# Performance work log

Measured on AMD Instinct MI355X. Metric: run time of the kernel, lower is better.

Reference implementation:

```python
import jax, jax.numpy as jnp
import numpy as np

INF = 1000000000.0
N_HEAD, QK, VD, NVAR = 4, 4, 4, 1


def _rope(xh, tf, thetas):
    # xh: [B, L, H, D], tf: [B, L], thetas: [D//2]
    freqs = tf[:, :, None] * thetas                     # [B, L, D//2]
    cos = jnp.cos(freqs)[:, :, None, :]                 # broadcast over heads
    sin = jnp.sin(freqs)[:, :, None, :]
    xr, xi = xh[..., 0::2], xh[..., 1::2]               # complex pairs
    out_r = xr * cos - xi * sin
    out_i = xr * sin + xi * cos
    return jnp.stack([out_r, out_i], axis=-1).reshape(xh.shape)


def setup_inputs() -> dict:
    key = jax.random.key(0)
    ks = jax.random.split(key, 11)
    bn, pn, pl = 32, 64, 128
    s = 0.1
    return {
        "x": jax.random.normal(ks[0], (bn, pn, pl), jnp.float32),
        "t": jax.random.uniform(ks[1], (bn, pn, pl), jnp.float32),
        "mask": jax.random.randint(ks[2], (bn, pn, pl), 0, 2, jnp.int32),
        "Wq": jax.random.normal(ks[3], (N_HEAD * QK, NVAR), jnp.float32) * s,
        "Wk": jax.random.normal(ks[4], (N_HEAD * QK, NVAR), jnp.float32) * s,
        "Wv": jax.random.normal(ks[5], (N_HEAD * VD, NVAR), jnp.float32) * s,
        "Wout": jax.random.normal(ks[6], (NVAR, N_HEAD * VD), jnp.float32) * s,
        "W1": jax.random.normal(ks[7], (4 * N_HEAD * VD, N_HEAD * VD), jnp.float32) * s,
        "b1": jnp.zeros((4 * N_HEAD * VD,), jnp.float32),
        "W2": jax.random.normal(ks[8], (N_HEAD * VD, 4 * N_HEAD * VD), jnp.float32) * s,
        "b2": jnp.zeros((N_HEAD * VD,), jnp.float32),
    }


def reference(x, t, mask, Wq, Wk, Wv, Wout, W1, b1, W2, b2):
    bn, pn, pl = x.shape
    B = bn * pn
    thetas = 1.0 / (1000.0 ** (jnp.arange(0, QK, 2, dtype=jnp.float32) / QK))
    x4 = x[..., None]                                       # [bn, pn, pl, 1]
    q = jnp.einsum('bpln,dn->bpld', x4, Wq).reshape(B, pl, N_HEAD, QK)
    k = jnp.einsum('bpln,dn->bpld', x4, Wk).reshape(B, pl, N_HEAD, QK)
    v = jnp.einsum('bpln,dn->bpld', x4, Wv).reshape(B, pl, N_HEAD, VD)
    tf = t.reshape(B, pl)
    q = _rope(q, tf, thetas)
    k = _rope(k, tf, thetas)
    q = q.transpose(0, 2, 1, 3)                             # [B, H, L, D]
    k = k.transpose(0, 2, 1, 3)
    v = v.transpose(0, 2, 1, 3)
    scale = QK ** 0.5
    attn = jnp.einsum('bhqd,bhkd->bhqk', q / scale, k)      # [B, H, L, L]
    m = mask.reshape(B, pl)
    mask_mat = (m[:, :, None] * m[:, None, :])[:, None, :, :]
    attn = jnp.where(mask_mat == 0, -INF, attn)
    attn = jax.nn.softmax(attn, axis=-1)
    o = jnp.einsum('bhqk,bhkd->bhqd', attn, v)
    o = o.transpose(0, 2, 1, 3).reshape(bn, pn, pl, N_HEAD * VD)
    ffn = jnp.maximum(o @ W1.T + b1, 0.0) @ W2.T + b2       # dropout off (eval)
    out_q = o + ffn
    return out_q @ Wout.T                                   # [bn, pn, pl, 1]
```

## Files before the change

kernel.cpp:

```cpp
#include <hip/hip_runtime.h>

constexpr int PL = 128;

typedef float f32x2 __attribute__((ext_vector_type(2)));

__device__ __forceinline__ float fast_exp2(float x) {
#if __has_builtin(__builtin_amdgcn_exp2f)
    return __builtin_amdgcn_exp2f(x);
#else
    return __expf(x * 0.69314718055994531f);
#endif
}
__device__ __forceinline__ f32x2 pk_fma(f32x2 a, f32x2 b, f32x2 c) {
    return __builtin_elementwise_fma(a, b, c);
}
__device__ __forceinline__ f32x2 sp(float v) { f32x2 r; r.x = v; r.y = v; return r; }

__global__ __launch_bounds__(256, 4) void fused_block_kernel(
    const float* __restrict__ x, const float* __restrict__ t, const int* __restrict__ mask,
    const float* __restrict__ Wq, const float* __restrict__ Wk, const float* __restrict__ Wv,
    const float* __restrict__ Wout, const float* __restrict__ W1, const float* __restrict__ b1,
    const float* __restrict__ W2, const float* __restrict__ b2,
    float* __restrict__ out)
{
    __shared__ float4 CSMc[2][64 * 3];
    __shared__ float4 ROWD[2][PL];
    __shared__ float  validR[2][PL];
    __shared__ f32x2  Gp[32][4];
    __shared__ __align__(8) float cg[64];
    __shared__ __align__(8) float b1s[64];
    __shared__ float  OST[2][4][PL];
    __shared__ float  xpart[2][2];
    __shared__ int    wcnt[2][2];
    __shared__ float  gwS[4];
    __shared__ float  bbS;

    const int tid  = threadIdx.x;
    const int blk  = blockIdx.x;
    const int seq  = tid >> 7;
    const int j    = tid & 127;
    const int lane = tid & 63;
    const int wh   = (tid >> 6) & 1;

    const float xv = x[(blk * 2 + seq) * PL + j];
    const float tv = t[(blk * 2 + seq) * PL + j];
    const int   mv = mask[(blk * 2 + seq) * PL + j];
    const float va = mv ? 1.0f : 0.0f;
    float xc0v, xs0v, xc1v, xs1v;
    {
        const float th1 = 0.031622776601683794f;
        xc0v = xv * __cosf(tv);        xs0v = xv * __sinf(tv);
        xc1v = xv * __cosf(tv * th1);  xs1v = xv * __sinf(tv * th1);
        ROWD[seq][j]   = make_float4(xc0v, xs0v, xc1v, xs1v);
        validR[seq][j] = va;
        float px = xv;
        #pragma unroll
        for (int off = 32; off >= 1; off >>= 1) px += __shfl_xor(px, off);
        if (lane == 0) xpart[seq][wh] = px;
    }
    const unsigned long long ball = __ballot(mv != 0);
    const int lpos = __popcll(ball & ((1ull << lane) - 1ull));
    if (lane == 0) wcnt[seq][wh] = __popcll(ball);

    if (tid < 64) {
        const int hid = tid;
        b1s[hid] = b1[hid];
        float c = 0.f;
        #pragma unroll
        for (int d = 0; d < 16; ++d) c += W2[d * 64 + hid] * Wout[d];
        cg[hid] = c;
        const float4* w1r = reinterpret_cast<const float4*>(W1 + hid * 16);
        #pragma unroll
        for (int h = 0; h < 4; ++h) {
            const float4 wv  = reinterpret_cast<const float4*>(Wv)[h];
            const float4 w1v = w1r[h];
            const float g = w1v.x*wv.x + w1v.y*wv.y + w1v.z*wv.z + w1v.w*wv.w;
            reinterpret_cast<float*>(&Gp[hid >> 1][h])[hid & 1] = g;
        }
    } else if (tid < 68) {
        const int h = tid - 64;
        const float4 wv = reinterpret_cast<const float4*>(Wv)[h];
        const float4 wo = reinterpret_cast<const float4*>(Wout)[h];
        gwS[h] = wv.x*wo.x + wv.y*wo.y + wv.z*wo.z + wv.w*wo.w;
    } else if (tid == 68) {
        float bb = 0.f;
        #pragma unroll
        for (int d = 0; d < 16; ++d) bb += b2[d] * Wout[d];
        bbS = bb;
    }
    __syncthreads();

    {
        float* C = reinterpret_cast<float*>(CSMc[seq]);
        const int pos = lpos + (wh ? wcnt[seq][0] : 0);
        if (mv) {
            const int p = pos >> 1, par = pos & 1;
            C[p*12 + 0 + par] = xc0v;
            C[p*12 + 2 + par] = xs0v;
            C[p*12 + 4 + par] = xc1v;
            C[p*12 + 6 + par] = xs1v;
            C[p*12 + 8 + par] = 1.0f;
            C[p*12 +10 + par] = xv;
        }
        const int nv = wcnt[seq][0] + wcnt[seq][1];
        if (j == 0 && (nv & 1)) {
            const int p = nv >> 1;
            C[p*12 + 1] = 0.f; C[p*12 + 3] = 0.f; C[p*12 + 5] = 0.f;
            C[p*12 + 7] = 0.f; C[p*12 + 9] = 0.f; C[p*12 +11] = 0.f;
        }
    }
    __syncthreads();

    {
        const int wave = tid >> 6;
        const int sq   = wave >> 1;
        const int hh   = wave & 1;
        const int l2   = tid & 63;
        const int h    = hh * 2 + (l2 >> 5);
        const int r0   = l2 & 31;
        const float4 wq4 = reinterpret_cast<const float4*>(Wq)[h];
        const float4 wk4 = reinterpret_cast<const float4*>(Wk)[h];
        const float a0  = wq4.x*wk4.x + wq4.y*wk4.y;
        const float be0 = wq4.x*wk4.y - wq4.y*wk4.x;
        const float a1  = wq4.z*wk4.z + wq4.w*wk4.w;
        const float be1 = wq4.z*wk4.w - wq4.w*wk4.z;
        const float gam = 0.5f * 1.4426950408889634f;

        f32x2 A[4], Bc[4], Cc[4], Dc[4], S[4], X[4];
        #pragma unroll
        for (int rr = 0; rr < 4; ++rr) {
            const int r = r0 + rr * 32;
            const float4 rd = ROWD[sq][r];
            A[rr]  = sp(gam * (rd.x * a0 + rd.y * be0));
            Bc[rr] = sp(gam * (rd.y * a0 - rd.x * be0));
            Cc[rr] = sp(gam * (rd.z * a1 + rd.w * be1));
            Dc[rr] = sp(gam * (rd.w * a1 - rd.z * be1));
            S[rr] = sp(0.f);
            X[rr] = sp(0.f);
        }
        const int nv    = wcnt[sq][0] + wcnt[sq][1];
        const int npair = (nv + 1) >> 1;
        #pragma unroll 2
        for (int jj = 0; jj < npair; ++jj) {
            const float4 ca = CSMc[sq][jj * 3 + 0];
            const float4 cb = CSMc[sq][jj * 3 + 1];
            const float4 mm = CSMc[sq][jj * 3 + 2];
            f32x2 c0p; c0p.x = ca.x; c0p.y = ca.y;
            f32x2 s0p; s0p.x = ca.z; s0p.y = ca.w;
            f32x2 c1p; c1p.x = cb.x; c1p.y = cb.y;
            f32x2 s1p; s1p.x = cb.z; s1p.y = cb.w;
            f32x2 vv;  vv.x  = mm.x; vv.y  = mm.y;
            f32x2 vx;  vx.x  = mm.z; vx.y  = mm.w;
            #pragma unroll
            for (int rr = 0; rr < 4; ++rr) {
                f32x2 L = A[rr] * c0p;
                L = pk_fma(Bc[rr], s0p, L);
                L = pk_fma(Cc[rr], c1p, L);
                L = pk_fma(Dc[rr], s1p, L);
                f32x2 E;
                E.x = fast_exp2(L.x);
                E.y = fast_exp2(L.y);
                S[rr] = pk_fma(E, vv, S[rr]);
                X[rr] = pk_fma(E, vx, X[rr]);
            }
        }
        const float sumx = xpart[sq][0] + xpart[sq][1];
        #pragma unroll
        for (int rr = 0; rr < 4; ++rr) {
            const int r = r0 + rr * 32;
            const float s  = S[rr].x + S[rr].y;
            const float wx = X[rr].x + X[rr].y;
            const bool  m  = validR[sq][r] != 0.f;
            OST[sq][h][r] = (m ? wx : sumx) / (m ? s : 128.f);
        }
    }
    __syncthreads();

    {
        const int qi = j;
        const float os0 = OST[seq][0][qi];
        const float os1 = OST[seq][1][qi];
        const float os2 = OST[seq][2][qi];
        const float os3 = OST[seq][3][qi];
        const f32x2* b1pair = reinterpret_cast<const f32x2*>(b1s);
        const f32x2* cgpair = reinterpret_cast<const f32x2*>(cg);
        const f32x2 q0 = sp(os0), q1 = sp(os1), q2 = sp(os2), q3 = sp(os3);
        f32x2 R2 = sp(0.f);
        #pragma unroll 8
        for (int p = 0; p < 32; ++p) {
            f32x2 HS = b1pair[p];
            HS = pk_fma(Gp[p][0], q0, HS);
            HS = pk_fma(Gp[p][1], q1, HS);
            HS = pk_fma(Gp[p][2], q2, HS);
            HS = pk_fma(Gp[p][3], q3, HS);
            HS.x = fmaxf(HS.x, 0.f);
            HS.y = fmaxf(HS.y, 0.f);
            R2 = pk_fma(cgpair[p], HS, R2);
        }
        const float r = R2.x + R2.y + bbS
                      + os0 * gwS[0] + os1 * gwS[1] + os2 * gwS[2] + os3 * gwS[3];
        out[(blk * 2 + seq) * PL + qi] = r;
    }
}

extern "C" void kernel_launch(void* const* d_in, const int* in_sizes, int n_in,
                              void* d_out, int out_size, void* d_ws, size_t ws_size,
                              hipStream_t stream) {
    const float* x    = (const float*)d_in[0];
    const float* t    = (const float*)d_in[1];
    const int*   mask = (const int*)d_in[2];
    const float* Wq   = (const float*)d_in[3];
    const float* Wk   = (const float*)d_in[4];
    const float* Wv   = (const float*)d_in[5];
    const float* Wout = (const float*)d_in[6];
    const float* W1   = (const float*)d_in[7];
    const float* b1   = (const float*)d_in[8];
    const float* W2   = (const float*)d_in[9];
    const float* b2   = (const float*)d_in[10];
    float* outp = (float*)d_out;
    const int B  = in_sizes[0] / PL;
    const int B2 = B / 2;
    fused_block_kernel<<<B2, 256, 0, stream>>>(x, t, mask, Wq, Wk, Wv, Wout, W1, b1, W2, b2, outp);
}
```

Measured before the change: 23.86 us.

## Compute attention only for valid query rows using compacted row indexing

Query rows now come from the compacted valid-token array, so attention is evaluated only for unmasked rows. When at most 64 rows are valid, a 2-row-per-thread specialization halves the exp/FMA work. Masked rows take the uniform mean value directly in the FFN stage. This removes the ROWD and validR shared buffers but adds a runtime branch between two template instantiations, which adds code size.

```diff
diff --git a/kernel.cpp b/kernel.cpp
--- a/kernel.cpp
+++ b/kernel.cpp
@@ -15,6 +15,60 @@
     return __builtin_elementwise_fma(a, b, c);
 }
 __device__ __forceinline__ f32x2 sp(float v) { f32x2 r; r.x = v; r.y = v; return r; }
+
+template <int NS>
+__device__ __forceinline__ void attn_core(
+    const float4* __restrict__ Cs, float* __restrict__ OSTc_h,
+    int npair, int nv, int r0,
+    float a0, float be0, float a1, float be1)
+{
+    const float gam = 0.5f * 1.4426950408889634f;
+    const float* Cf = reinterpret_cast<const float*>(Cs);
+    f32x2 A[NS], Bc[NS], Cc[NS], Dc[NS], S[NS], X[NS];
+    #pragma unroll
+    for (int rr = 0; rr < NS; ++rr) {
+        const int i = r0 + rr * 32;
+        const int p = i >> 1, par = i & 1;
+        const float xc0 = Cf[p*12 + 0 + par], xs0 = Cf[p*12 + 2 + par];
+        const float xc1 = Cf[p*12 + 4 + par], xs1 = Cf[p*12 + 6 + par];
+        A[rr]  = sp(gam * (xc0 * a0 + xs0 * be0));
+        Bc[rr] = sp(gam * (xs0 * a0 - xc0 * be0));
+        Cc[rr] = sp(gam * (xc1 * a1 + xs1 * be1));
+        Dc[rr] = sp(gam * (xs1 * a1 - xc1 * be1));
+        S[rr]  = sp(0.f);
+        X[rr]  = sp(0.f);
+    }
+    #pragma unroll 2
+    for (int jj = 0; jj < npair; ++jj) {
+        const float4 ca = Cs[jj * 3 + 0];
+        const float4 cb = Cs[jj * 3 + 1];
+        const float4 mm = Cs[jj * 3 + 2];
+        f32x2 c0p; c0p.x = ca.x; c0p.y = ca.y;
+        f32x2 s0p; s0p.x = ca.z; s0p.y = ca.w;
+        f32x2 c1p; c1p.x = cb.x; c1p.y = cb.y;
+        f32x2 s1p; s1p.x = cb.z; s1p.y = cb.w;
+        f32x2 vv;  vv.x  = mm.x; vv.y  = mm.y;
+        f32x2 vx;  vx.x  = mm.z; vx.y  = mm.w;
+        #pragma unroll
+        for (int rr = 0; rr < NS; ++rr) {
+            f32x2 L = A[rr] * c0p;
+            L = pk_fma(Bc[rr], s0p, L);
+            L = pk_fma(Cc[rr], c1p, L);
+            L = pk_fma(Dc[rr], s1p, L);
+            f32x2 E;
+            E.x = fast_exp2(L.x);
+            E.y = fast_exp2(L.y);
+            S[rr] = pk_fma(E, vv, S[rr]);
+            X[rr] = pk_fma(E, vx, X[rr]);
+        }
+    }
+    #pragma unroll
+    for (int rr = 0; rr < NS; ++rr) {
+        const int i = r0 + rr * 32;
+        if (i < nv)
+            OSTc_h[i] = (X[rr].x + X[rr].y) / (S[rr].x + S[rr].y);
+    }
+}
 
 __global__ __launch_bounds__(256, 4) void fused_block_kernel(
     const float* __restrict__ x, const float* __restrict__ t, const int* __restrict__ mask,
@@ -24,12 +78,10 @@
     float* __restrict__ out)
 {
     __shared__ float4 CSMc[2][64 * 3];
-    __shared__ float4 ROWD[2][PL];
-    __shared__ float  validR[2][PL];
     __shared__ f32x2  Gp[32][4];
     __shared__ __align__(8) float cg[64];
     __shared__ __align__(8) float b1s[64];
-    __shared__ float  OST[2][4][PL];
+    __shared__ float  OSTc[2][4][PL];
     __shared__ float  xpart[2][2];
     __shared__ int    wcnt[2][2];
     __shared__ float  gwS[4];
@@ -45,14 +97,11 @@
     const float xv = x[(blk * 2 + seq) * PL + j];
     const float tv = t[(blk * 2 + seq) * PL + j];
     const int   mv = mask[(blk * 2 + seq) * PL + j];
-    const float va = mv ? 1.0f : 0.0f;
     float xc0v, xs0v, xc1v, xs1v;
     {
         const float th1 = 0.031622776601683794f;
         xc0v = xv * __cosf(tv);        xs0v = xv * __sinf(tv);
         xc1v = xv * __cosf(tv * th1);  xs1v = xv * __sinf(tv * th1);
-        ROWD[seq][j]   = make_float4(xc0v, xs0v, xc1v, xs1v);
-        validR[seq][j] = va;
         float px = xv;
         #pragma unroll
         for (int off = 32; off >= 1; off >>= 1) px += __shfl_xor(px, off);
@@ -90,9 +139,9 @@
     }
     __syncthreads();
 
+    const int pos = lpos + (wh ? wcnt[seq][0] : 0);
     {
         float* C = reinterpret_cast<float*>(CSMc[seq]);
-        const int pos = lpos + (wh ? wcnt[seq][0] : 0);
         if (mv) {
             const int p = pos >> 1, par = pos & 1;
             C[p*12 + 0 + par] = xc0v;
@@ -124,64 +173,29 @@
         const float be0 = wq4.x*wk4.y - wq4.y*wk4.x;
         const float a1  = wq4.z*wk4.z + wq4.w*wk4.w;
         const float be1 = wq4.z*wk4.w - wq4.w*wk4.z;
-        const float gam = 0.5f * 1.4426950408889634f;
-
-        f32x2 A[4], Bc[4], Cc[4], Dc[4], S[4], X[4];
-        #pragma unroll
-        for (int rr = 0; rr < 4; ++rr) {
-            const int r = r0 + rr * 32;
-            const float4 rd = ROWD[sq][r];
-            A[rr]  = sp(gam * (rd.x * a0 + rd.y * be0));
-            Bc[rr] = sp(gam * (rd.y * a0 - rd.x * be0));
-            Cc[rr] = sp(gam * (rd.z * a1 + rd.w * be1));
-            Dc[rr] = sp(gam * (rd.w * a1 - rd.z * be1));
-            S[rr] = sp(0.f);
-            X[rr] = sp(0.f);
-        }
+
         const int nv    = wcnt[sq][0] + wcnt[sq][1];
         const int npair = (nv + 1) >> 1;
-        #pragma unroll 2
-        for (int jj = 0; jj < npair; ++jj) {
-            const float4 ca = CSMc[sq][jj * 3 + 0];
-            const float4 cb = CSMc[sq][jj * 3 + 1];
-            const float4 mm = CSMc[sq][jj * 3 + 2];
-            f32x2 c0p; c0p.x = ca.x; c0p.y = ca.y;
-            f32x2 s0p; s0p.x = ca.z; s0p.y = ca.w;
-            f32x2 c1p; c1p.x = cb.x; c1p.y = cb.y;
-            f32x2 s1p; s1p.x = cb.z; s1p.y = cb.w;
-            f32x2 vv;  vv.x  = mm.x; vv.y  = mm.y;
-            f32x2 vx;  vx.x  = mm.z; vx.y  = mm.w;
-            #pragma unroll
-            for (int rr = 0; rr < 4; ++rr) {
-                f32x2 L = A[rr] * c0p;
-                L = pk_fma(Bc[rr], s0p, L);
-                L = pk_fma(Cc[rr], c1p, L);
-                L = pk_fma(Dc[rr], s1p, L);
-                f32x2 E;
-                E.x = fast_exp2(L.x);
-                E.y = fast_exp2(L.y);
-                S[rr] = pk_fma(E, vv, S[rr]);
-                X[rr] = pk_fma(E, vx, X[rr]);
-            }
-        }
-        const float sumx = xpart[sq][0] + xpart[sq][1];
-        #pragma unroll
-        for (int rr = 0; rr < 4; ++rr) {
-            const int r = r0 + rr * 32;
-            const float s  = S[rr].x + S[rr].y;
-            const float wx = X[rr].x + X[rr].y;
-            const bool  m  = validR[sq][r] != 0.f;
-            OST[sq][h][r] = (m ? wx : sumx) / (m ? s : 128.f);
-        }
+        const float4* Cs = CSMc[sq];
+        float* oh = &OSTc[sq][h][0];
+        if (nv <= 64)
+            attn_core<2>(Cs, oh, npair, nv, r0, a0, be0, a1, be1);
+        else
+            attn_core<4>(Cs, oh, npair, nv, r0, a0, be0, a1, be1);
     }
     __syncthreads();
 
     {
-        const int qi = j;
-        const float os0 = OST[seq][0][qi];
-        const float os1 = OST[seq][1][qi];
-        const float os2 = OST[seq][2][qi];
-        const float os3 = OST[seq][3][qi];
+        const float sm = (xpart[seq][0] + xpart[seq][1]) * (1.0f / 128.0f);
+        float os0, os1, os2, os3;
+        if (mv) {
+            os0 = OSTc[seq][0][pos];
+            os1 = OSTc[seq][1][pos];
+            os2 = OSTc[seq][2][pos];
+            os3 = OSTc[seq][3][pos];
+        } else {
+            os0 = os1 = os2 = os3 = sm;
+        }
         const f32x2* b1pair = reinterpret_cast<const f32x2*>(b1s);
         const f32x2* cgpair = reinterpret_cast<const f32x2*>(cg);
         const f32x2 q0 = sp(os0), q1 = sp(os1), q2 = sp(os2), q3 = sp(os3);
@@ -199,7 +213,7 @@
         }
         const float r = R2.x + R2.y + bbS
                       + os0 * gwS[0] + os1 * gwS[1] + os2 * gwS[2] + os3 * gwS[3];
-        out[(blk * 2 + seq) * PL + qi] = r;
+        out[(blk * 2 + seq) * PL + j] = r;
     }
 }
 
```

Result: no change. 24.18 us (+1.3%).
